# Kernel optimization log

Measured on AMD Instinct MI355X. Metric: run time of the kernel, lower is better.

Reference implementation:

```python
import jax, jax.numpy as jnp
import numpy as np

MEM, KEY, VAL, DIN, BS, BQ = 1000, 64, 128, 512, 512, 65536


def setup_inputs() -> dict:
    key = jax.random.key(0)
    ks = jax.random.split(key, 20)

    def lin(k, fan_in, shape):
        return (jax.random.normal(k, shape, jnp.float32) / np.sqrt(fan_in)).astype(jnp.float32)

    return {
        "support_x": jax.random.normal(ks[0], (BS, DIN), jnp.float32),
        "support_y": jax.random.normal(ks[1], (BS, VAL), jnp.float32),
        "query_x": jax.random.normal(ks[2], (BQ, DIN), jnp.float32),
        "query_y": jax.random.normal(ks[3], (BQ, 1), jnp.float32),
        # base model: Linear(DIN -> KEY)
        "base_W": lin(ks[4], DIN, (DIN, KEY)),
        "base_b": jnp.zeros((KEY,), jnp.float32),
        # ExternalMemory projections
        "kp_W": lin(ks[5], KEY, (KEY, KEY)),
        "kp_b": jnp.zeros((KEY,), jnp.float32),
        "vp_W": lin(ks[6], VAL, (VAL, VAL)),
        "vp_b": jnp.zeros((VAL,), jnp.float32),
        # memory buffers (randn keys/values like register_buffer(torch.randn))
        "mem_keys": jax.random.normal(ks[7], (MEM, KEY), jnp.float32),
        "mem_values": jax.random.normal(ks[8], (MEM, VAL), jnp.float32),
        # ages: uniform so top-k picks distinct slots deterministically
        "mem_age": jax.random.uniform(ks[9], (MEM,), jnp.float32),
        # controller MLP: Linear(KEY+VAL,128) ReLU Linear(128,64) ReLU Linear(64,1)
        "c1_W": lin(ks[10], KEY + VAL, (KEY + VAL, 128)),
        "c1_b": jnp.zeros((128,), jnp.float32),
        "c2_W": lin(ks[11], 128, (128, 64)),
        "c2_b": jnp.zeros((64,), jnp.float32),
        "c3_W": lin(ks[12], 64, (64, 1)),
        "c3_b": jnp.zeros((1,), jnp.float32),
    }


def reference(support_x, support_y, query_x, query_y,
              base_W, base_b, kp_W, kp_b, vp_W, vp_b,
              mem_keys, mem_values, mem_age,
              c1_W, c1_b, c2_W, c2_b, c3_W, c3_b):
    # base model features
    support_feat = support_x @ base_W + base_b          # [BS, KEY]
    query_feat = query_x @ base_W + base_b              # [BQ, KEY]

    # --- memory.write(support_feat, support_y) ---
    proj_keys = support_feat @ kp_W + kp_b              # [BS, KEY]
    proj_vals = support_y @ vp_W + vp_b                 # [BS, VAL]
    _, oldest = jax.lax.top_k(mem_age, BS)              # evict oldest BS slots
    new_keys = mem_keys.at[oldest].set(proj_keys)       # [MEM, KEY]
    new_values = mem_values.at[oldest].set(proj_vals)   # [MEM, VAL]

    # --- memory.read(query_feat) ---
    proj_q = query_feat @ kp_W + kp_b                   # [BQ, KEY]
    sims = proj_q @ new_keys.T                          # [BQ, MEM]
    attn = jax.nn.softmax(sims, axis=-1)
    retrieved = attn @ new_values                       # [BQ, VAL]

    # --- controller MLP on [query_feat ; retrieved] ---
    aug = jnp.concatenate([query_feat, retrieved], axis=-1)  # [BQ, KEY+VAL]
    h = jax.nn.relu(aug @ c1_W + c1_b)
    h = jax.nn.relu(h @ c2_W + c2_b)
    query_pred = h @ c3_W + c3_b                        # [BQ, 1]

    meta_loss = jnp.mean((query_pred - query_y) ** 2)
    return meta_loss, query_pred, retrieved
```

## Files before the change

kernel.cpp:

```cpp
#include <hip/hip_runtime.h>

typedef _Float16 h8v __attribute__((ext_vector_type(8)));
typedef _Float16 h4v __attribute__((ext_vector_type(4)));
typedef float    f4v __attribute__((ext_vector_type(4)));

#define MFMA16(a,b,c) __builtin_amdgcn_mfma_f32_16x16x32_f16((a),(b),(c),0,0,0)
#define NEGF (-1e30f)

#define MEM 1000
#define KEY 64
#define VAL 128
#define DIN 512
#define BS  512
#define BQ  65536


typedef __attribute__((address_space(1))) const unsigned int guint;
typedef __attribute__((address_space(3))) unsigned int luint;

__device__ __forceinline__ void gld16(const _Float16* g, _Float16* l)
{
  __builtin_amdgcn_global_load_lds((guint*)g, (luint*)l, 16, 0, 0);
}

__device__ __forceinline__ h8v cvt8(const float* p)
{
  f4v u = *(const f4v*)p;
  f4v v = *(const f4v*)(p + 4);
  h8v a;
  a[0] = (_Float16)u.x; a[1] = (_Float16)u.y; a[2] = (_Float16)u.z; a[3] = (_Float16)u.w;
  a[4] = (_Float16)v.x; a[5] = (_Float16)v.y; a[6] = (_Float16)v.z; a[7] = (_Float16)v.w;
  return a;
}

__device__ __forceinline__ h8v cvt8nt(const float* p)
{
  f4v u = __builtin_nontemporal_load((const f4v*)p);
  f4v v = __builtin_nontemporal_load((const f4v*)(p + 4));
  h8v a;
  a[0] = (_Float16)u.x; a[1] = (_Float16)u.y; a[2] = (_Float16)u.z; a[3] = (_Float16)u.w;
  a[4] = (_Float16)v.x; a[5] = (_Float16)v.y; a[6] = (_Float16)v.z; a[7] = (_Float16)v.w;
  return a;
}

__global__ void k_prep1(const float* __restrict__ baseW, const float* __restrict__ base_b,
                        const float* __restrict__ kpW, const float* __restrict__ kp_b,
                        const float* __restrict__ vpW, const float* __restrict__ c1W,
                        const float* __restrict__ c2W, const float* __restrict__ age,
                        _Float16* __restrict__ WTf, float* __restrict__ bcomb,
                        _Float16* __restrict__ vpWt, _Float16* __restrict__ c1F,
                        _Float16* __restrict__ c2F, int* __restrict__ ranks,
                        float* __restrict__ out0)
{
  long id = (long)blockIdx.x * 256 + threadIdx.x;
  if (id < 65536) {
    int h = (int)id;
    int j = h & 7, lane = (h >> 3) & 63, KS = (h >> 9) & 15, F = h >> 13;
    int n = F * 16 + (lane & 15);
    int k = KS * 32 + ((lane >> 4) << 3) + j;
    float v;
    if (n < 64) v = baseW[(size_t)k * 64 + n];
    else {
      int nn = n - 64;
      const float* br = baseW + (size_t)k * 64;
      float s = 0.f;
      for (int t = 0; t < 64; ++t) s += br[t] * kpW[t * 64 + nn];
      v = s;
    }
    WTf[h] = (_Float16)v;
  } else if (id < 65664) {
    int i = (int)(id - 65536);
    if (i < 64) bcomb[i] = base_b[i];
    else {
      int n = i - 64;
      float s = kp_b[n];
      for (int t = 0; t < 64; ++t) s += base_b[t] * kpW[t * 64 + n];
      bcomb[i] = s;
    }
  } else if (id < 90240) {
    int h = (int)(id - 65664);
    int j = h & 7, lane = (h >> 3) & 63, KS = (h >> 9) % 6, F = (h >> 9) / 6;
    int n = F * 16 + (lane & 15);
    int k = KS * 32 + ((lane >> 4) << 3) + j;
    c1F[h] = (_Float16)c1W[(size_t)k * 128 + n];
  } else if (id < 98432) {
    int h = (int)(id - 90240);
    int j = h & 7, lane = (h >> 3) & 63, KS = (h >> 9) & 3, F = h >> 11;
    int n = F * 16 + (lane & 15);
    int k = KS * 32 + ((lane >> 4) << 3) + j;
    c2F[h] = (_Float16)c2W[(size_t)k * 64 + n];
  } else if (id < 114816) {
    long i = id - 98432;
    int n = (int)(i >> 7), k = (int)(i & 127);
    vpWt[i] = (_Float16)vpW[(size_t)k * 128 + n];
  } else if (id < 115816) {
    int jx = (int)(id - 114816);
    float aj = age[jx];
    int r = 0;
    for (int i2 = 0; i2 < MEM; ++i2) {
      float ai = age[i2];
      r += (ai > aj) || (ai == aj && i2 < jx);
    }
    ranks[jx] = r;
  } else if (id == 115816) {
    *out0 = 0.f;
  }
}

__global__ __launch_bounds__(64) void k_prep2(
    const float* __restrict__ sx, const float* __restrict__ sy,
    const _Float16* __restrict__ WTf, const float* __restrict__ bcomb,
    const _Float16* __restrict__ vpWt, const float* __restrict__ vp_b,
    float* __restrict__ pkeys, float* __restrict__ pvals)
{
  const int lane = threadIdx.x, quad = lane >> 4, l15 = lane & 15;
  const f4v fz = {0.f, 0.f, 0.f, 0.f};
  if (blockIdx.x < 32) {
    const int m0 = blockIdx.x * 16;
    f4v acc[4];
    #pragma unroll
    for (int f = 0; f < 4; ++f) acc[f] = fz;
    const float* xr = sx + (size_t)(m0 + l15) * DIN;
    #pragma unroll 4
    for (int ks = 0; ks < 16; ++ks) {
      int k0 = ks * 32 + quad * 8;
      h8v a = cvt8(xr + k0);
      #pragma unroll
      for (int f = 0; f < 4; ++f) {
        h8v b = *(const h8v*)(WTf + (size_t)((((4 + f) * 16) + ks) * 64 + lane) * 8);
        acc[f] = MFMA16(a, b, acc[f]);
      }
    }
    #pragma unroll
    for (int f = 0; f < 4; ++f) {
      int col = f * 16 + l15;
      float bb = bcomb[64 + col];
      #pragma unroll
      for (int r = 0; r < 4; ++r)
        pkeys[(size_t)(m0 + quad * 4 + r) * KEY + col] = acc[f][r] + bb;
    }
  } else {
    const int m0 = (blockIdx.x - 32) * 16;
    f4v acc[8];
    #pragma unroll
    for (int f = 0; f < 8; ++f) acc[f] = fz;
    const float* yr = sy + (size_t)(m0 + l15) * VAL;
    #pragma unroll
    for (int ks = 0; ks < 4; ++ks) {
      int k0 = ks * 32 + quad * 8;
      h8v a = cvt8(yr + k0);
      #pragma unroll
      for (int f = 0; f < 8; ++f) {
        h8v b = *(const h8v*)(vpWt + (size_t)(f * 16 + l15) * 128 + k0);
        acc[f] = MFMA16(a, b, acc[f]);
      }
    }
    #pragma unroll
    for (int f = 0; f < 8; ++f) {
      int col = f * 16 + l15;
      float bb = vp_b[col];
      #pragma unroll
      for (int r = 0; r < 4; ++r)
        pvals[(size_t)(m0 + quad * 4 + r) * VAL + col] = acc[f][r] + bb;
    }
  }
}

__global__ void k_prep3(const int* __restrict__ ranks, const float* __restrict__ pk,
                        const float* __restrict__ pv, const float* __restrict__ memK,
                        const float* __restrict__ memV,
                        _Float16* __restrict__ keysF, _Float16* __restrict__ valF)
{
  int id = blockIdx.x * 256 + threadIdx.x;
  if (id < 65536) {
    int j = id & 7, lane = (id >> 3) & 63, KS = (id >> 9) & 1, F = id >> 10;
    int n = F * 16 + (lane & 15);
    int k = KS * 32 + ((lane >> 4) << 3) + j;
    float v = 0.f;
    if (n < MEM) {
      int rk = ranks[n];
      v = (rk < BS) ? pk[(size_t)rk * KEY + k] : memK[(size_t)n * KEY + k];
    }
    keysF[id] = (_Float16)v;
  } else {
    int h = id - 65536;
    int j = h & 7, lane = (h >> 3) & 63, KS = (h >> 9) & 31, F = h >> 14;
    int nv = F * 16 + (lane & 15);
    int jm = KS * 32 + ((j >> 2) << 4) + (((lane >> 4)) << 2) + (j & 3);
    float v = 0.f;
    if (jm < MEM) {
      int rk = ranks[jm];
      v = (rk < BS) ? pv[(size_t)rk * VAL + nv] : memV[(size_t)jm * VAL + nv];
    }
    valF[h] = (_Float16)v;
  }
}


#define SM_PV(S, rm, rl, O, Vc, c)                                          \
  {                                                                         \
    float cm = NEGF;                                                        \
    _Pragma("unroll")                                                       \
    for (int f = 0; f < 8; ++f) {                                           \
      const int sb = (c) * 128 + f * 16 + quad * 4;                         \
      _Pragma("unroll")                                                     \
      for (int r = 0; r < 4; ++r) {                                         \
        float s = (sb + r < MEM) ? S[f][r] : NEGF;                          \
        S[f][r] = s;                                                        \
        cm = fmaxf(cm, s);                                                  \
      }                                                                     \
    }                                                                       \
    cm = fmaxf(cm, __shfl_xor(cm, 16));                                     \
    cm = fmaxf(cm, __shfl_xor(cm, 32));                                     \
    float mn = fmaxf(rm, cm);                                               \
    float al = __expf(rm - mn);                                             \
    rm = mn;                                                                \
    float psl = 0.f;                                                        \
    _Pragma("unroll")                                                       \
    for (int f = 0; f < 8; ++f)                                             \
      _Pragma("unroll")                                                     \
      for (int r = 0; r < 4; ++r) {                                         \
        float p = __expf(S[f][r] - mn);                                     \
        S[f][r] = p;                                                        \
        psl += p;                                                           \
      }                                                                     \
    rl = rl * al + psl;                                                     \
    float alO[4];                                                           \
    _Pragma("unroll")                                                       \
    for (int r = 0; r < 4; ++r) alO[r] = __shfl(al, quad * 4 + r);          \
    _Pragma("unroll")                                                       \
    for (int v = 0; v < 8; ++v)                                             \
      _Pragma("unroll")                                                     \
      for (int r = 0; r < 4; ++r) O[v][r] *= alO[r];                        \
    _Pragma("unroll")                                                       \
    for (int ks = 0; ks < 4; ++ks) {                                        \
      h8v a;                                                                \
      _Pragma("unroll")                                                     \
      for (int e = 0; e < 4; ++e) {                                         \
        a[e]     = (_Float16)S[2 * ks][e];                                  \
        a[e + 4] = (_Float16)S[2 * ks + 1][e];                              \
      }                                                                     \
      _Pragma("unroll")                                                     \
      for (int v = 0; v < 8; ++v) {                                         \
        h8v b = *(const h8v*)(Vc + (size_t)(v * 4 + ks) * 512 + lane * 8);  \
        O[v] = MFMA16(a, b, O[v]);                                          \
      }                                                                     \
    }                                                                       \
  }

__global__ __launch_bounds__(512, 2) void k_fused(
    const float* __restrict__ qx, const float* __restrict__ qy,
    const _Float16* __restrict__ WTf, const float* __restrict__ bcomb,
    const float* __restrict__ c1_b, const float* __restrict__ c2_b,
    const float* __restrict__ c3W, const float* __restrict__ c3b,
    const _Float16* __restrict__ c1F, const _Float16* __restrict__ c2F,
    const _Float16* __restrict__ keysF, const _Float16* __restrict__ valF,
    float* __restrict__ dout)
{
  __shared__ __align__(16) char smem[151552];
  _Float16* const WTsh = (_Float16*)smem;
  _Float16* const K0   = (_Float16*)smem;
  _Float16* const K1   = (_Float16*)(smem + 16384);
  _Float16* const V0   = (_Float16*)(smem + 32768);
  _Float16* const V1   = (_Float16*)(smem + 65536);

  const int tid  = threadIdx.x;
  const int wid  = tid >> 6;
  const int lane = tid & 63;
  const int quad = lane >> 4;
  const int l15  = lane & 15;

  _Float16* const P_s  = (_Float16*)(smem + 98304 + wid * 6656);
  _Float16* const h2_s = P_s + 2176;

  const int tile = blockIdx.x * 8 + wid;
  const int q0   = tile * 16;

  float* out_pred = dout + 1;
  float* out_ret  = dout + 1 + BQ;
  const f4v fz = {0.f, 0.f, 0.f, 0.f};

  #pragma unroll
  for (int i = 0; i < 16; ++i) {
    const int t = wid * 16 + i;
    gld16(WTf + (size_t)t * 512 + lane * 8, WTsh + t * 512);
  }
  asm volatile("s_waitcnt vmcnt(0)" ::: "memory");
  __syncthreads();

  f4v acc[8];
  #pragma unroll
  for (int f = 0; f < 8; ++f) acc[f] = fz;
  const float* xr = qx + (size_t)(q0 + l15) * DIN;

  #pragma unroll 4
  for (int ks = 0; ks < 16; ++ks) {
    const int k0 = ks * 32 + quad * 8;
    h8v a = cvt8nt(xr + k0);
    #pragma unroll
    for (int f = 0; f < 8; ++f) {
      h8v b = *(const h8v*)(WTsh + (size_t)((f * 16 + ks) * 64 + lane) * 8);
      acc[f] = MFMA16(a, b, acc[f]);
    }
  }
  __syncthreads();

  _Float16* tbuf = (_Float16*)(smem + wid * 4352);
  h8v pq0, pq1;
  {
    #pragma unroll
    for (int f = 0; f < 8; ++f) {
      float bb = bcomb[f * 16 + l15];
      #pragma unroll
      for (int r = 0; r < 4; ++r)
        tbuf[(quad * 4 + r) * 136 + f * 16 + l15] = (_Float16)(acc[f][r] + bb);
    }
    h8v qf0 = *(const h8v*)&tbuf[l15 * 136 +  0 + quad * 8];
    h8v qf1 = *(const h8v*)&tbuf[l15 * 136 + 32 + quad * 8];
    pq0 = *(const h8v*)&tbuf[l15 * 136 + 64 + quad * 8];
    pq1 = *(const h8v*)&tbuf[l15 * 136 + 96 + quad * 8];
    *(h8v*)&P_s[0 * 512 + lane * 8] = qf0;
    *(h8v*)&P_s[1 * 512 + lane * 8] = qf1;
  }
  __syncthreads();

  #pragma unroll
  for (int i = 0; i < 2; ++i) {
    const int t = wid * 2 + i;
    gld16(keysF + (size_t)t * 512 + lane * 8, K0 + t * 512);
  }
  #pragma unroll
  for (int i = 0; i < 4; ++i) {
    const int t = wid * 4 + i;
    const int v = t >> 2, sub = t & 3;
    gld16(valF + ((size_t)(v * 32 + sub)) * 512 + lane * 8,
          V0 + (v * 4 + sub) * 512);
  }
  asm volatile("s_waitcnt vmcnt(0)" ::: "memory");
  __syncthreads();

  float rm = NEGF, rl = 0.f;
  f4v O[8];
  #pragma unroll
  for (int v = 0; v < 8; ++v) O[v] = fz;

  #pragma unroll 1
  for (int c = 0; c < 8; ++c) {
    const int cur = c & 1;
    _Float16* const Kc = cur ? K1 : K0;
    _Float16* const Vc = cur ? V1 : V0;
    _Float16* const Kn = cur ? K0 : K1;
    _Float16* const Vn = cur ? V0 : V1;

    if (c < 7) {
      const int nc = c + 1;
      const _Float16* kc = keysF + (size_t)nc * 8192;
      #pragma unroll
      for (int i = 0; i < 2; ++i) {
        const int t = wid * 2 + i;
        gld16(kc + (size_t)t * 512 + lane * 8, Kn + t * 512);
      }
      #pragma unroll
      for (int i = 0; i < 4; ++i) {
        const int t = wid * 4 + i;
        const int v = t >> 2, sub = t & 3;
        gld16(valF + ((size_t)(v * 32 + nc * 4 + sub)) * 512 + lane * 8,
              Vn + (v * 4 + sub) * 512);
      }
    } else {
      #pragma unroll
      for (int i = 0; i < 6; ++i) {
        const int t = wid * 6 + i;
        _Float16* dst = (t < 16) ? (K0 + t * 512) : (V0 + (t - 16) * 512);
        gld16(c1F + (size_t)t * 512 + lane * 8, dst);
      }
    }

    {
      f4v S[8];
      #pragma unroll
      for (int f = 0; f < 8; ++f) S[f] = fz;
      #pragma unroll
      for (int f = 0; f < 8; ++f) {
        h8v b0 = *(const h8v*)(Kc + (size_t)(f * 2 + 0) * 512 + lane * 8);
        h8v b1 = *(const h8v*)(Kc + (size_t)(f * 2 + 1) * 512 + lane * 8);
        S[f] = MFMA16(b0, pq0, S[f]);
        S[f] = MFMA16(b1, pq1, S[f]);
      }
      SM_PV(S, rm, rl, O, Vc, c)
    }

    asm volatile("s_waitcnt vmcnt(0)" ::: "memory");
    __syncthreads();
  }

  rl += __shfl_xor(rl, 16); rl += __shfl_xor(rl, 32);
  float rlO[4];
  #pragma unroll
  for (int r = 0; r < 4; ++r) rlO[r] = __shfl(rl, quad * 4 + r);

  h8v qf0 = *(const h8v*)&P_s[0 * 512 + lane * 8];
  h8v qf1 = *(const h8v*)&P_s[1 * 512 + lane * 8];

  #pragma unroll
  for (int v = 0; v < 8; ++v)
    #pragma unroll
    for (int r = 0; r < 4; ++r)
      P_s[(quad * 4 + r) * 136 + v * 16 + l15] = (_Float16)(O[v][r] / rlO[r]);

  #pragma unroll
  for (int it = 0; it < 8; ++it) {
    int flat = it * 256 + lane * 4;
    int row = flat >> 7, col = flat & 127;
    h4v t = *(const h4v*)&P_s[row * 136 + col];
    f4v o;
    o.x = (float)t[0]; o.y = (float)t[1]; o.z = (float)t[2]; o.w = (float)t[3];
    __builtin_nontemporal_store(o, (f4v*)(out_ret + (size_t)q0 * VAL + flat));
  }

  {
    f4v H[8];
    #pragma unroll
    for (int f = 0; f < 8; ++f) H[f] = fz;
    #pragma unroll
    for (int ks = 0; ks < 6; ++ks) {
      const int k0 = ks * 32;
      h8v a = (ks == 0) ? qf0 : (ks == 1) ? qf1
               : *(const h8v*)&P_s[l15 * 136 + (k0 - 64) + quad * 8];
      #pragma unroll
      for (int f = 0; f < 8; ++f) {
        const int t = f * 6 + ks;
        const _Float16* bp = (t < 16) ? (K0 + (size_t)t * 512)
                                      : (V0 + (size_t)(t - 16) * 512);
        h8v b = *(const h8v*)(bp + lane * 8);
        H[f] = MFMA16(a, b, H[f]);
      }
    }
    #pragma unroll
    for (int f = 0; f < 8; ++f) {
      float bb = c1_b[f * 16 + l15];
      #pragma unroll
      for (int r = 0; r < 4; ++r)
        P_s[(quad * 4 + r) * 136 + f * 16 + l15] =
            (_Float16)fmaxf(0.f, H[f][r] + bb);
    }
  }

  {
    f4v G[4];
    #pragma unroll
    for (int f = 0; f < 4; ++f) G[f] = fz;
    #pragma unroll
    for (int ks = 0; ks < 4; ++ks) {
      h8v a = *(const h8v*)&P_s[l15 * 136 + ks * 32 + quad * 8];
      #pragma unroll
      for (int f = 0; f < 4; ++f) {
        h8v b = *(const h8v*)(c2F + (size_t)(f * 4 + ks) * 512 + lane * 8);
        G[f] = MFMA16(a, b, G[f]);
      }
    }
    #pragma unroll
    for (int f = 0; f < 4; ++f) {
      float bb = c2_b[f * 16 + l15];
      #pragma unroll
      for (int r = 0; r < 4; ++r)
        h2_s[(quad * 4 + r) * 72 + f * 16 + l15] =
            (_Float16)fmaxf(0.f, G[f][r] + bb);
    }
  }

  float lsum;
  {
    const int prow = lane >> 2, pj = lane & 3;
    float s = 0.f;
    #pragma unroll
    for (int k = 0; k < 16; ++k) {
      int kk = pj * 16 + k;
      s += (float)h2_s[prow * 72 + kk] * c3W[kk];
    }
    s += __shfl_xor(s, 1);
    s += __shfl_xor(s, 2);
    float pred = s + c3b[0];
    float diff = pred - qy[q0 + prow];
    if (pj == 0) out_pred[q0 + prow] = pred;
    lsum = diff * diff;
  }
  #pragma unroll
  for (int m = 1; m < 64; m <<= 1) lsum += __shfl_xor(lsum, m);
  if (lane == 0) atomicAdd(dout, lsum * (1.0f / (4.0f * (float)BQ)));
}

extern "C" void kernel_launch(void* const* d_in, const int* in_sizes, int n_in,
                              void* d_out, int out_size, void* d_ws, size_t ws_size,
                              hipStream_t stream)
{
  const float* support_x = (const float*)d_in[0];
  const float* support_y = (const float*)d_in[1];
  const float* query_x   = (const float*)d_in[2];
  const float* query_y   = (const float*)d_in[3];
  const float* base_W    = (const float*)d_in[4];
  const float* base_b    = (const float*)d_in[5];
  const float* kp_W      = (const float*)d_in[6];
  const float* kp_b      = (const float*)d_in[7];
  const float* vp_W      = (const float*)d_in[8];
  const float* vp_b      = (const float*)d_in[9];
  const float* mem_keys  = (const float*)d_in[10];
  const float* mem_vals  = (const float*)d_in[11];
  const float* mem_age   = (const float*)d_in[12];
  const float* c1_W      = (const float*)d_in[13];
  const float* c1_b      = (const float*)d_in[14];
  const float* c2_W      = (const float*)d_in[15];
  const float* c2_b      = (const float*)d_in[16];
  const float* c3_W      = (const float*)d_in[17];
  const float* c3_b      = (const float*)d_in[18];

  char* w = (char*)d_ws;
  _Float16* WTf   = (_Float16*)(w + 0);
  _Float16* vpWt  = (_Float16*)(w + 131072);
  _Float16* c1F   = (_Float16*)(w + 163840);
  _Float16* c2F   = (_Float16*)(w + 212992);
  float*    bcomb = (float*)   (w + 229376);
  int*      ranks = (int*)     (w + 229888);
  float*    pkeys = (float*)   (w + 233984);
  float*    pvals = (float*)   (w + 365056);
  _Float16* keysF = (_Float16*)(w + 627200);
  _Float16* valF  = (_Float16*)(w + 758272);

  float* out = (float*)d_out;

  hipLaunchKernelGGL(k_prep1, dim3(453), dim3(256), 0, stream,
                     base_W, base_b, kp_W, kp_b, vp_W, c1_W, c2_W, mem_age,
                     WTf, bcomb, vpWt, c1F, c2F, ranks, out);
  hipLaunchKernelGGL(k_prep2, dim3(64), dim3(64), 0, stream,
                     support_x, support_y, WTf, bcomb, vpWt, vp_b, pkeys, pvals);
  hipLaunchKernelGGL(k_prep3, dim3(768), dim3(256), 0, stream,
                     ranks, pkeys, pvals, mem_keys, mem_vals, keysF, valF);
  hipLaunchKernelGGL(k_fused, dim3(BQ / 128), dim3(512), 0, stream,
                     query_x, query_y, WTf, bcomb, c1_b, c2_b, c3_W, c3_b,
                     c1F, c2F, keysF, valF, out);
}
```

Before: 363.0 us.

## Shrink LDS footprint to raise occupancy with smaller staged tiles

Cuts shared memory from about 148KB to 64KB and raises launch bounds from 2 to 4 blocks per CU. To fit, the base-weight projection now streams the weights in four double-buffered quarters instead of staging all of them at once. The key/value loop is split into 16 chunks of 64 instead of 8 chunks of 128, and the c1 weights are read straight from global memory. The aim is more resident waves to hide latency, at the cost of more barriers, smaller MFMA batches per chunk, uncached global reads for c1, and tighter register limits that could cause spills.

New measurement: 370.3 us. 1.02x slower.

```diff
diff --git a/kernel.cpp b/kernel.cpp
--- a/kernel.cpp
+++ b/kernel.cpp
@@ -196,59 +196,7 @@
   }
 }
 
-
-#define SM_PV(S, rm, rl, O, Vc, c)                                          \
-  {                                                                         \
-    float cm = NEGF;                                                        \
-    _Pragma("unroll")                                                       \
-    for (int f = 0; f < 8; ++f) {                                           \
-      const int sb = (c) * 128 + f * 16 + quad * 4;                         \
-      _Pragma("unroll")                                                     \
-      for (int r = 0; r < 4; ++r) {                                         \
-        float s = (sb + r < MEM) ? S[f][r] : NEGF;                          \
-        S[f][r] = s;                                                        \
-        cm = fmaxf(cm, s);                                                  \
-      }                                                                     \
-    }                                                                       \
-    cm = fmaxf(cm, __shfl_xor(cm, 16));                                     \
-    cm = fmaxf(cm, __shfl_xor(cm, 32));                                     \
-    float mn = fmaxf(rm, cm);                                               \
-    float al = __expf(rm - mn);                                             \
-    rm = mn;                                                                \
-    float psl = 0.f;                                                        \
-    _Pragma("unroll")                                                       \
-    for (int f = 0; f < 8; ++f)                                             \
-      _Pragma("unroll")                                                     \
-      for (int r = 0; r < 4; ++r) {                                         \
-        float p = __expf(S[f][r] - mn);                                     \
-        S[f][r] = p;                                                        \
-        psl += p;                                                           \
-      }                                                                     \
-    rl = rl * al + psl;                                                     \
-    float alO[4];                                                           \
-    _Pragma("unroll")                                                       \
-    for (int r = 0; r < 4; ++r) alO[r] = __shfl(al, quad * 4 + r);          \
-    _Pragma("unroll")                                                       \
-    for (int v = 0; v < 8; ++v)                                             \
-      _Pragma("unroll")                                                     \
-      for (int r = 0; r < 4; ++r) O[v][r] *= alO[r];                        \
-    _Pragma("unroll")                                                       \
-    for (int ks = 0; ks < 4; ++ks) {                                        \
-      h8v a;                                                                \
-      _Pragma("unroll")                                                     \
-      for (int e = 0; e < 4; ++e) {                                         \
-        a[e]     = (_Float16)S[2 * ks][e];                                  \
-        a[e + 4] = (_Float16)S[2 * ks + 1][e];                              \
-      }                                                                     \
-      _Pragma("unroll")                                                     \
-      for (int v = 0; v < 8; ++v) {                                         \
-        h8v b = *(const h8v*)(Vc + (size_t)(v * 4 + ks) * 512 + lane * 8);  \
-        O[v] = MFMA16(a, b, O[v]);                                          \
-      }                                                                     \
-    }                                                                       \
-  }
-
-__global__ __launch_bounds__(512, 2) void k_fused(
+__global__ __launch_bounds__(512, 4) void k_fused(
     const float* __restrict__ qx, const float* __restrict__ qy,
     const _Float16* __restrict__ WTf, const float* __restrict__ bcomb,
     const float* __restrict__ c1_b, const float* __restrict__ c2_b,
@@ -257,12 +205,13 @@
     const _Float16* __restrict__ keysF, const _Float16* __restrict__ valF,
     float* __restrict__ dout)
 {
-  __shared__ __align__(16) char smem[151552];
-  _Float16* const WTsh = (_Float16*)smem;
-  _Float16* const K0   = (_Float16*)smem;
-  _Float16* const K1   = (_Float16*)(smem + 16384);
-  _Float16* const V0   = (_Float16*)(smem + 32768);
-  _Float16* const V1   = (_Float16*)(smem + 65536);
+  __shared__ __align__(16) char smem[65536];
+  _Float16* const Wq0 = (_Float16*)smem;
+  _Float16* const Wq1 = (_Float16*)(smem + 32768);
+  _Float16* const K0 = (_Float16*)smem;
+  _Float16* const K1 = (_Float16*)(smem + 8192);
+  _Float16* const V0 = (_Float16*)(smem + 16384);
+  _Float16* const V1 = (_Float16*)(smem + 32768);
 
   const int tid  = threadIdx.x;
   const int wid  = tid >> 6;
@@ -270,7 +219,8 @@
   const int quad = lane >> 4;
   const int l15  = lane & 15;
 
-  _Float16* const P_s  = (_Float16*)(smem + 98304 + wid * 6656);
+  _Float16* const qstash = (_Float16*)(smem + 49152 + wid * 2048);
+  _Float16* const P_s  = (_Float16*)(smem + wid * 6656);
   _Float16* const h2_s = P_s + 2176;
 
   const int tile = blockIdx.x * 8 + wid;
@@ -281,9 +231,10 @@
   const f4v fz = {0.f, 0.f, 0.f, 0.f};
 
   #pragma unroll
-  for (int i = 0; i < 16; ++i) {
-    const int t = wid * 16 + i;
-    gld16(WTf + (size_t)t * 512 + lane * 8, WTsh + t * 512);
+  for (int i = 0; i < 4; ++i) {
+    const int t = wid * 4 + i;
+    const int f = t >> 2, ksq = t & 3;
+    gld16(WTf + (size_t)(f * 16 + ksq) * 512 + lane * 8, Wq0 + t * 512);
   }
   asm volatile("s_waitcnt vmcnt(0)" ::: "memory");
   __syncthreads();
@@ -293,17 +244,32 @@
   for (int f = 0; f < 8; ++f) acc[f] = fz;
   const float* xr = qx + (size_t)(q0 + l15) * DIN;
 
-  #pragma unroll 4
-  for (int ks = 0; ks < 16; ++ks) {
-    const int k0 = ks * 32 + quad * 8;
-    h8v a = cvt8nt(xr + k0);
-    #pragma unroll
-    for (int f = 0; f < 8; ++f) {
-      h8v b = *(const h8v*)(WTsh + (size_t)((f * 16 + ks) * 64 + lane) * 8);
-      acc[f] = MFMA16(a, b, acc[f]);
-    }
-  }
-  __syncthreads();
+  #pragma unroll
+  for (int q = 0; q < 4; ++q) {
+    _Float16* const Wb = (q & 1) ? Wq1 : Wq0;
+    _Float16* const Wn = (q & 1) ? Wq0 : Wq1;
+    if (q < 3) {
+      #pragma unroll
+      for (int i = 0; i < 4; ++i) {
+        const int t = wid * 4 + i;
+        const int f = t >> 2, ksq = t & 3;
+        gld16(WTf + (size_t)(f * 16 + (q + 1) * 4 + ksq) * 512 + lane * 8,
+              Wn + t * 512);
+      }
+    }
+    #pragma unroll
+    for (int ksq = 0; ksq < 4; ++ksq) {
+      const int ks = q * 4 + ksq;
+      h8v a = cvt8nt(xr + ks * 32 + quad * 8);
+      #pragma unroll
+      for (int f = 0; f < 8; ++f) {
+        h8v b = *(const h8v*)(Wb + (size_t)((f * 4 + ksq) * 64 + lane) * 8);
+        acc[f] = MFMA16(a, b, acc[f]);
+      }
+    }
+    asm volatile("s_waitcnt vmcnt(0)" ::: "memory");
+    __syncthreads();
+  }
 
   _Float16* tbuf = (_Float16*)(smem + wid * 4352);
   h8v pq0, pq1;
@@ -319,22 +285,20 @@
     h8v qf1 = *(const h8v*)&tbuf[l15 * 136 + 32 + quad * 8];
     pq0 = *(const h8v*)&tbuf[l15 * 136 + 64 + quad * 8];
     pq1 = *(const h8v*)&tbuf[l15 * 136 + 96 + quad * 8];
-    *(h8v*)&P_s[0 * 512 + lane * 8] = qf0;
-    *(h8v*)&P_s[1 * 512 + lane * 8] = qf1;
+    *(h8v*)&qstash[0 * 512 + lane * 8] = qf0;
+    *(h8v*)&qstash[1 * 512 + lane * 8] = qf1;
   }
   __syncthreads();
 
   #pragma unroll
-  for (int i = 0; i < 2; ++i) {
-    const int t = wid * 2 + i;
-    gld16(keysF + (size_t)t * 512 + lane * 8, K0 + t * 512);
-  }
-  #pragma unroll
-  for (int i = 0; i < 4; ++i) {
-    const int t = wid * 4 + i;
-    const int v = t >> 2, sub = t & 3;
-    gld16(valF + ((size_t)(v * 32 + sub)) * 512 + lane * 8,
-          V0 + (v * 4 + sub) * 512);
+  for (int i = 0; i < 3; ++i) {
+    const int t = wid * 3 + i;
+    if (t < 8) gld16(keysF + (size_t)t * 512 + lane * 8, K0 + t * 512);
+    else {
+      const int tv = t - 8;
+      gld16(valF + (size_t)((tv >> 1) * 32 + (tv & 1)) * 512 + lane * 8,
+            V0 + tv * 512);
+    }
   }
   asm volatile("s_waitcnt vmcnt(0)" ::: "memory");
   __syncthreads();
@@ -345,49 +309,86 @@
   for (int v = 0; v < 8; ++v) O[v] = fz;
 
   #pragma unroll 1
-  for (int c = 0; c < 8; ++c) {
+  for (int c = 0; c < 16; ++c) {
     const int cur = c & 1;
     _Float16* const Kc = cur ? K1 : K0;
     _Float16* const Vc = cur ? V1 : V0;
     _Float16* const Kn = cur ? K0 : K1;
     _Float16* const Vn = cur ? V0 : V1;
 
-    if (c < 7) {
+    if (c < 15) {
       const int nc = c + 1;
-      const _Float16* kc = keysF + (size_t)nc * 8192;
-      #pragma unroll
-      for (int i = 0; i < 2; ++i) {
-        const int t = wid * 2 + i;
-        gld16(kc + (size_t)t * 512 + lane * 8, Kn + t * 512);
-      }
-      #pragma unroll
-      for (int i = 0; i < 4; ++i) {
-        const int t = wid * 4 + i;
-        const int v = t >> 2, sub = t & 3;
-        gld16(valF + ((size_t)(v * 32 + nc * 4 + sub)) * 512 + lane * 8,
-              Vn + (v * 4 + sub) * 512);
-      }
-    } else {
-      #pragma unroll
-      for (int i = 0; i < 6; ++i) {
-        const int t = wid * 6 + i;
-        _Float16* dst = (t < 16) ? (K0 + t * 512) : (V0 + (t - 16) * 512);
-        gld16(c1F + (size_t)t * 512 + lane * 8, dst);
-      }
-    }
-
-    {
-      f4v S[8];
-      #pragma unroll
-      for (int f = 0; f < 8; ++f) S[f] = fz;
-      #pragma unroll
-      for (int f = 0; f < 8; ++f) {
-        h8v b0 = *(const h8v*)(Kc + (size_t)(f * 2 + 0) * 512 + lane * 8);
-        h8v b1 = *(const h8v*)(Kc + (size_t)(f * 2 + 1) * 512 + lane * 8);
-        S[f] = MFMA16(b0, pq0, S[f]);
-        S[f] = MFMA16(b1, pq1, S[f]);
-      }
-      SM_PV(S, rm, rl, O, Vc, c)
+      #pragma unroll
+      for (int i = 0; i < 3; ++i) {
+        const int t = wid * 3 + i;
+        if (t < 8)
+          gld16(keysF + (size_t)(nc * 8 + t) * 512 + lane * 8, Kn + t * 512);
+        else {
+          const int tv = t - 8;
+          gld16(valF + (size_t)((tv >> 1) * 32 + nc * 2 + (tv & 1)) * 512 + lane * 8,
+                Vn + tv * 512);
+        }
+      }
+    }
+
+    f4v S[4];
+    #pragma unroll
+    for (int f = 0; f < 4; ++f) S[f] = fz;
+    #pragma unroll
+    for (int f = 0; f < 4; ++f) {
+      h8v b0 = *(const h8v*)(Kc + (size_t)(f * 2 + 0) * 512 + lane * 8);
+      h8v b1 = *(const h8v*)(Kc + (size_t)(f * 2 + 1) * 512 + lane * 8);
+      S[f] = MFMA16(b0, pq0, S[f]);
+      S[f] = MFMA16(b1, pq1, S[f]);
+    }
+
+    float cm = NEGF;
+    #pragma unroll
+    for (int f = 0; f < 4; ++f) {
+      const int sb = c * 64 + f * 16 + quad * 4;
+      #pragma unroll
+      for (int r = 0; r < 4; ++r) {
+        float s = (sb + r < MEM) ? S[f][r] : NEGF;
+        S[f][r] = s;
+        cm = fmaxf(cm, s);
+      }
+    }
+    cm = fmaxf(cm, __shfl_xor(cm, 16));
+    cm = fmaxf(cm, __shfl_xor(cm, 32));
+    float mn = fmaxf(rm, cm);
+    float al = __expf(rm - mn);
+    rm = mn;
+    float psl = 0.f;
+    #pragma unroll
+    for (int f = 0; f < 4; ++f)
+      #pragma unroll
+      for (int r = 0; r < 4; ++r) {
+        float p = __expf(S[f][r] - mn);
+        S[f][r] = p;
+        psl += p;
+      }
+    rl = rl * al + psl;
+    float alO[4];
+    #pragma unroll
+    for (int r = 0; r < 4; ++r) alO[r] = __shfl(al, quad * 4 + r);
+    #pragma unroll
+    for (int v = 0; v < 8; ++v)
+      #pragma unroll
+      for (int r = 0; r < 4; ++r) O[v][r] *= alO[r];
+
+    #pragma unroll
+    for (int ks2 = 0; ks2 < 2; ++ks2) {
+      h8v a;
+      #pragma unroll
+      for (int e = 0; e < 4; ++e) {
+        a[e]     = (_Float16)S[2 * ks2][e];
+        a[e + 4] = (_Float16)S[2 * ks2 + 1][e];
+      }
+      #pragma unroll
+      for (int v = 0; v < 8; ++v) {
+        h8v b = *(const h8v*)(Vc + (size_t)(v * 2 + ks2) * 512 + lane * 8);
+        O[v] = MFMA16(a, b, O[v]);
+      }
     }
 
     asm volatile("s_waitcnt vmcnt(0)" ::: "memory");
@@ -399,8 +400,9 @@
   #pragma unroll
   for (int r = 0; r < 4; ++r) rlO[r] = __shfl(rl, quad * 4 + r);
 
-  h8v qf0 = *(const h8v*)&P_s[0 * 512 + lane * 8];
-  h8v qf1 = *(const h8v*)&P_s[1 * 512 + lane * 8];
+  h8v qf0 = *(const h8v*)&qstash[0 * 512 + lane * 8];
+  h8v qf1 = *(const h8v*)&qstash[1 * 512 + lane * 8];
+  __syncthreads();
 
   #pragma unroll
   for (int v = 0; v < 8; ++v)
@@ -429,10 +431,7 @@
                : *(const h8v*)&P_s[l15 * 136 + (k0 - 64) + quad * 8];
       #pragma unroll
       for (int f = 0; f < 8; ++f) {
-        const int t = f * 6 + ks;
-        const _Float16* bp = (t < 16) ? (K0 + (size_t)t * 512)
-                                      : (V0 + (size_t)(t - 16) * 512);
-        h8v b = *(const h8v*)(bp + lane * 8);
+        h8v b = *(const h8v*)(c1F + (size_t)(f * 6 + ks) * 512 + lane * 8);
         H[f] = MFMA16(a, b, H[f]);
       }
     }
```
